# Optimization experiments

Measured on AMD Instinct MI355X. Metric: run time of the kernel, lower is better.

The kernel has to match this reference:

```python
import jax, jax.numpy as jnp
import numpy as np

GRID_SIZE = 10
DEGREE = 3


def bspline_basis(x, grid_size=GRID_SIZE, degree=DEGREE):
    """Cox-de Boor B-spline basis on a uniform grid over [-1, 1].
    x: (...,) -> (..., grid_size + degree)
    """
    h = 2.0 / grid_size
    # extended knot vector, length grid_size + 2*degree + 1
    knots = jnp.arange(-degree, grid_size + degree + 1, dtype=x.dtype) * h - 1.0
    # keep inputs inside the grid support (standard KAN practice)
    x = jnp.clip(x, -1.0, 1.0 - 1e-6)
    xe = x[..., None]
    b = ((xe >= knots[:-1]) & (xe < knots[1:])).astype(x.dtype)  # degree-0, (..., K-1)
    for d in range(1, degree + 1):
        left = (xe - knots[: -(d + 1)]) / (knots[d:-1] - knots[: -(d + 1)]) * b[..., :-1]
        right = (knots[d + 1:] - xe) / (knots[d + 1:] - knots[1:-d]) * b[..., 1:]
        b = left + right
    return b  # (..., grid_size + degree)


def setup_inputs() -> dict:
    key = jax.random.key(0)
    k1, k2, k3 = jax.random.split(key, 3)
    B, S, IN, OUT, E = 4, 2048, 256, 256, 8
    n_basis = GRID_SIZE + DEGREE
    x = jax.random.normal(k1, (B, S, IN), dtype=jnp.float32)
    coeff = jax.random.normal(k2, (E, n_basis), dtype=jnp.float32) * 0.1
    gating_weights = jax.random.normal(k3, (IN, OUT, E), dtype=jnp.float32)
    return {"x": x, "coeff": coeff, "gating_weights": gating_weights}


def reference(x, coeff, gating_weights):
    # spline experts: elementwise basis eval, then per-expert linear combo
    basis = bspline_basis(x)                              # (B, S, I, n_basis)
    expert_outputs = jnp.einsum('bsin,en->bsie', basis, coeff)  # (B, S, I, E)
    gates = jax.nn.softmax(gating_weights, axis=-1)       # (I, O, E)
    out = jnp.einsum('bsie,ioe->bso', expert_outputs, gates)
    return out
```

## Files before the change

kernel.cpp:

```cpp
#include <hip/hip_runtime.h>

typedef __attribute__((ext_vector_type(8))) short short8;
typedef __attribute__((ext_vector_type(4))) float f32x4;

#define IN_DIM 256
#define OUT_DIM 256
#define NB 16
#define KDIM (IN_DIM * NB)
#define TM 128
#define TN 128
#define BK 64
#define LDA 72
#define KSPLIT 2
#define IPER (IN_DIM / KSPLIT)
#define STEPS (IPER / 4)
#define XPITCH 129
#define XBYTES (TM * XPITCH * 4)
#define ABYTES (TM * LDA * 2)
#define LDS_TOTAL (XBYTES + 4 * ABYTES)

__device__ __forceinline__ unsigned short f2bf(float f) {
  union { float f; unsigned int u; } v; v.f = f;
  unsigned int r = v.u + 0x7fffu + ((v.u >> 16) & 1u);
  return (unsigned short)(r >> 16);
}

__device__ __forceinline__ void spline_row(float xv, unsigned short* rowp) {
  float xc = fminf(fmaxf(xv, -1.0f), 1.0f - 1e-6f);
  float u = (xc + 1.0f) * 5.0f;
  int c = (int)u;
  c = c > 9 ? 9 : (c < 0 ? 0 : c);
  float tt = u - (float)c;
  float omt = 1.0f - tt;
  float t2 = tt * tt, t3 = t2 * tt;
  float b0 = omt * omt * omt * (1.0f / 6.0f);
  float b1 = (3.0f * t3 - 6.0f * t2 + 4.0f) * (1.0f / 6.0f);
  float b2 = (-3.0f * t3 + 3.0f * t2 + 3.0f * tt + 1.0f) * (1.0f / 6.0f);
  float b3 = t3 * (1.0f / 6.0f);
  unsigned h0 = f2bf(b0), h1 = f2bf(b1), h2 = f2bf(b2), h3 = f2bf(b3);
  const int a = c >> 1;
  const bool odd = (c & 1) != 0;
  unsigned p01 = h0 | (h1 << 16);
  unsigned p23 = h2 | (h3 << 16);
  unsigned A0 = odd ? (h0 << 16) : p01;
  unsigned A1 = odd ? (h1 | (h2 << 16)) : p23;
  unsigned A2 = odd ? h3 : 0u;
  unsigned d[8];
#pragma unroll
  for (int j = 0; j < 8; ++j) {
    unsigned v = (j == a) ? A0 : 0u;
    v = (j == a + 1) ? A1 : v;
    v = (j == a + 2) ? A2 : v;
    d[j] = v;
  }
  *(int4*)&rowp[0] = *(const int4*)&d[0];
  *(int4*)&rowp[8] = *(const int4*)&d[4];
}

__global__ __launch_bounds__(256) void kan_prep(const float* __restrict__ coeff,
                                                const float* __restrict__ gw,
                                                unsigned short* __restrict__ BmT,
                                                float* __restrict__ out) {
  __shared__ float csh[104];
  __shared__ unsigned short tile[16][256];
  const int t = threadIdx.x;
  {
    const int bid = blockIdx.y * 16 + blockIdx.x;
    float4 z; z.x = z.y = z.z = z.w = 0.f;
    float4* ob = (float4*)out;
#pragma unroll
    for (int j = 0; j < 8; ++j) ob[(size_t)bid * 2048 + j * 256 + t] = z;
  }
  if (t < 104) csh[t] = coeff[t];
  __syncthreads();
  const int otile = blockIdx.x, itile = blockIdx.y;
  const int il = t >> 4, ol = t & 15;
  const int i = itile * 16 + il;
  const int o = otile * 16 + ol;
  const float* g = gw + (size_t)(i * OUT_DIM + o) * 8;
  float4 g0 = *(const float4*)g;
  float4 g1 = *(const float4*)(g + 4);
  float ge[8] = {g0.x, g0.y, g0.z, g0.w, g1.x, g1.y, g1.z, g1.w};
  float mx = ge[0];
#pragma unroll
  for (int e = 1; e < 8; ++e) mx = fmaxf(mx, ge[e]);
  float p[8]; float s = 0.f;
#pragma unroll
  for (int e = 0; e < 8; ++e) { p[e] = __expf(ge[e] - mx); s += p[e]; }
  const float inv = 1.0f / s;
  unsigned short row[16];
#pragma unroll
  for (int n = 0; n < 13; ++n) {
    float w = 0.f;
#pragma unroll
    for (int e = 0; e < 8; ++e) w += p[e] * csh[e * 13 + n];
    row[n] = f2bf(w * inv);
  }
  row[13] = 0; row[14] = 0; row[15] = 0;
  int4* dst = (int4*)&tile[ol][il * 16];
  dst[0] = *(const int4*)&row[0];
  dst[1] = *(const int4*)&row[8];
  __syncthreads();
  const int oo = t >> 4, ck = t & 15;
  int4 v0 = *(const int4*)&tile[oo][ck * 16];
  int4 v1 = *(const int4*)&tile[oo][ck * 16 + 8];
  int4* out4 = (int4*)(BmT + (size_t)(otile * 16 + oo) * KDIM + itile * 256 + ck * 16);
  out4[0] = v0;
  out4[1] = v1;
}

__global__ __launch_bounds__(256, 1) void kan_gemm(const float* __restrict__ x,
                                                   const unsigned short* __restrict__ BmT,
                                                   float* __restrict__ out) {
  extern __shared__ char lds_raw[];
  float* Xsh = (float*)lds_raw;
  unsigned short* AshB = (unsigned short*)(lds_raw + XBYTES);
  unsigned short* BshB = AshB + 2 * TM * LDA;

  const int t = threadIdx.x;
  const int lane = t & 63;
  const int wave = t >> 6;
  const int wm = wave & 1, wn = wave >> 1;
  const int mb = blockIdx.x * TM;
  const int ob = blockIdx.y * TN;
  const int i0 = blockIdx.z * IPER;

  const int mloc = t & 127;
  const int il0 = t >> 7;

  {
    const int xr = t >> 5;
    const int xc = t & 31;
#pragma unroll
    for (int p = 0; p < 16; ++p) {
      const int r = xr + 8 * p;
      float4 v = *(const float4*)(x + (size_t)(mb + r) * IN_DIM + i0 + xc * 4);
      float* d = Xsh + r * XPITCH + xc * 4;
      d[0] = v.x; d[1] = v.y; d[2] = v.z; d[3] = v.w;
    }
  }

  const unsigned short* bsrc[4];
  int bdst[4];
#pragma unroll
  for (int r = 0; r < 4; ++r) {
    int olo = (t >> 3) + 32 * r;
    bsrc[r] = BmT + (size_t)(ob + olo) * KDIM + i0 * NB + (t & 7) * 8;
    bdst[r] = olo * LDA + (t & 7) * 8;
  }

  int4 breg[4];
#pragma unroll
  for (int r = 0; r < 4; ++r) breg[r] = *(const int4*)(bsrc[r]);

  f32x4 acc[4][4];
#pragma unroll
  for (int a = 0; a < 4; ++a)
#pragma unroll
    for (int b = 0; b < 4; ++b) acc[a][b] = (f32x4){0.f, 0.f, 0.f, 0.f};

  int aoff[4], boff[4];
#pragma unroll
  for (int f = 0; f < 4; ++f) {
    aoff[f] = (wm * 64 + f * 16 + (lane & 15)) * LDA + (lane >> 4) * 8;
    boff[f] = (wn * 64 + f * 16 + (lane & 15)) * LDA + (lane >> 4) * 8;
  }

  __syncthreads();

  {
#pragma unroll
    for (int r = 0; r < 4; ++r) *(int4*)&BshB[bdst[r]] = breg[r];
#pragma unroll
    for (int rr = 0; rr < 2; ++rr) {
      const int il = il0 + 2 * rr;
      spline_row(Xsh[mloc * XPITCH + il], AshB + mloc * LDA + il * NB);
    }
  }

  for (int s = 0; s < STEPS; ++s) {
    __syncthreads();
    const int cur = s & 1;
    const bool more = (s + 1 < STEPS);
    if (more) {
#pragma unroll
      for (int r = 0; r < 4; ++r) breg[r] = *(const int4*)(bsrc[r] + (s + 1) * BK);
    }
    const unsigned short* Ac = AshB + cur * (TM * LDA);
    const unsigned short* Bc = BshB + cur * (TN * LDA);
#pragma unroll
    for (int kc = 0; kc < 2; ++kc) {
      short8 af[4], bfr[4];
#pragma unroll
      for (int f = 0; f < 4; ++f) af[f] = *(const short8*)&Ac[aoff[f] + kc * 32];
#pragma unroll
      for (int f = 0; f < 4; ++f) bfr[f] = *(const short8*)&Bc[boff[f] + kc * 32];
#pragma unroll
      for (int mf = 0; mf < 4; ++mf)
#pragma unroll
        for (int nf = 0; nf < 4; ++nf)
          acc[mf][nf] = __builtin_amdgcn_mfma_f32_16x16x32_bf16(af[mf], bfr[nf], acc[mf][nf], 0, 0, 0);
    }
    if (more) {
      unsigned short* An = AshB + (1 - cur) * (TM * LDA);
      unsigned short* Bn = BshB + (1 - cur) * (TN * LDA);
#pragma unroll
      for (int r = 0; r < 4; ++r) *(int4*)&Bn[bdst[r]] = breg[r];
#pragma unroll
      for (int rr = 0; rr < 2; ++rr) {
        const int il = il0 + 2 * rr;
        spline_row(Xsh[mloc * XPITCH + (s + 1) * 4 + il], An + mloc * LDA + il * NB);
      }
    }
  }

#pragma unroll
  for (int mf = 0; mf < 4; ++mf)
#pragma unroll
    for (int nf = 0; nf < 4; ++nf)
#pragma unroll
      for (int r = 0; r < 4; ++r) {
        int row = mb + wm * 64 + mf * 16 + ((lane >> 4) << 2) + r;
        int col = ob + wn * 64 + nf * 16 + (lane & 15);
        atomicAdd(out + (size_t)row * OUT_DIM + col, acc[mf][nf][r]);
      }
}

extern "C" void kernel_launch(void* const* d_in, const int* in_sizes, int n_in,
                              void* d_out, int out_size, void* d_ws, size_t ws_size,
                              hipStream_t stream) {
  const float* x     = (const float*)d_in[0];
  const float* coeff = (const float*)d_in[1];
  const float* gw    = (const float*)d_in[2];
  float* out = (float*)d_out;
  unsigned short* BmT = (unsigned short*)d_ws;

  hipFuncSetAttribute((const void*)kan_gemm,
                      hipFuncAttributeMaxDynamicSharedMemorySize, LDS_TOTAL);
  kan_prep<<<dim3(16, 16), dim3(256), 0, stream>>>(coeff, gw, BmT, out);
  dim3 grid(8192 / TM, OUT_DIM / TN, KSPLIT);
  kan_gemm<<<grid, dim3(256), LDS_TOTAL, stream>>>(x, BmT, out);
}
```

Measured before the change: 127.4 us.

## Drop LDS x staging, stream x per step, raise K-split and occupancy

Removes the large per-block shared-memory staging of x and instead loads two x values per thread from global memory each pipeline step, prefetched alongside the B tile. This shrinks LDS to the A/B double buffers only, which lets launch bounds request two blocks per CU. The K split is also doubled to 4 to create more blocks. The cost is more global atomics into the output and smaller, less coalesced per-step x loads.

```diff
diff --git a/kernel.cpp b/kernel.cpp
--- a/kernel.cpp
+++ b/kernel.cpp
@@ -11,13 +11,9 @@
 #define TN 128
 #define BK 64
 #define LDA 72
-#define KSPLIT 2
+#define KSPLIT 4
 #define IPER (IN_DIM / KSPLIT)
 #define STEPS (IPER / 4)
-#define XPITCH 129
-#define XBYTES (TM * XPITCH * 4)
-#define ABYTES (TM * LDA * 2)
-#define LDS_TOTAL (XBYTES + 4 * ABYTES)
 
 __device__ __forceinline__ unsigned short f2bf(float f) {
   union { float f; unsigned int u; } v; v.f = f;
@@ -109,13 +105,11 @@
   out4[1] = v1;
 }
 
-__global__ __launch_bounds__(256, 1) void kan_gemm(const float* __restrict__ x,
+__global__ __launch_bounds__(256, 2) void kan_gemm(const float* __restrict__ x,
                                                    const unsigned short* __restrict__ BmT,
                                                    float* __restrict__ out) {
-  extern __shared__ char lds_raw[];
-  float* Xsh = (float*)lds_raw;
-  unsigned short* AshB = (unsigned short*)(lds_raw + XBYTES);
-  unsigned short* BshB = AshB + 2 * TM * LDA;
+  __shared__ unsigned short AshB[2][TM * LDA];
+  __shared__ unsigned short BshB[2][TN * LDA];
 
   const int t = threadIdx.x;
   const int lane = t & 63;
@@ -125,33 +119,19 @@
   const int ob = blockIdx.y * TN;
   const int i0 = blockIdx.z * IPER;
 
-  const int mloc = t & 127;
-  const int il0 = t >> 7;
-
-  {
-    const int xr = t >> 5;
-    const int xc = t & 31;
-#pragma unroll
-    for (int p = 0; p < 16; ++p) {
-      const int r = xr + 8 * p;
-      float4 v = *(const float4*)(x + (size_t)(mb + r) * IN_DIM + i0 + xc * 4);
-      float* d = Xsh + r * XPITCH + xc * 4;
-      d[0] = v.x; d[1] = v.y; d[2] = v.z; d[3] = v.w;
-    }
-  }
+  const int r = t & 127;
+  const int ph = t >> 7;
+  const float* xrow = x + (size_t)(mb + r) * IN_DIM + i0 + 2 * ph;
+  const int adst = r * LDA + 2 * ph * NB;
 
   const unsigned short* bsrc[4];
   int bdst[4];
 #pragma unroll
-  for (int r = 0; r < 4; ++r) {
-    int olo = (t >> 3) + 32 * r;
-    bsrc[r] = BmT + (size_t)(ob + olo) * KDIM + i0 * NB + (t & 7) * 8;
-    bdst[r] = olo * LDA + (t & 7) * 8;
-  }
-
-  int4 breg[4];
-#pragma unroll
-  for (int r = 0; r < 4; ++r) breg[r] = *(const int4*)(bsrc[r]);
+  for (int q = 0; q < 4; ++q) {
+    int olo = (t >> 3) + 32 * q;
+    bsrc[q] = BmT + (size_t)(ob + olo) * KDIM + i0 * NB + (t & 7) * 8;
+    bdst[q] = olo * LDA + (t & 7) * 8;
+  }
 
   f32x4 acc[4][4];
 #pragma unroll
@@ -166,28 +146,30 @@
     boff[f] = (wn * 64 + f * 16 + (lane & 15)) * LDA + (lane >> 4) * 8;
   }
 
-  __syncthreads();
-
   {
-#pragma unroll
-    for (int r = 0; r < 4; ++r) *(int4*)&BshB[bdst[r]] = breg[r];
-#pragma unroll
-    for (int rr = 0; rr < 2; ++rr) {
-      const int il = il0 + 2 * rr;
-      spline_row(Xsh[mloc * XPITCH + il], AshB + mloc * LDA + il * NB);
-    }
+    float2 x0 = *(const float2*)xrow;
+    int4 breg[4];
+#pragma unroll
+    for (int q = 0; q < 4; ++q) breg[q] = *(const int4*)(bsrc[q]);
+#pragma unroll
+    for (int q = 0; q < 4; ++q) *(int4*)&BshB[0][bdst[q]] = breg[q];
+    spline_row(x0.x, &AshB[0][adst]);
+    spline_row(x0.y, &AshB[0][adst + NB]);
   }
 
   for (int s = 0; s < STEPS; ++s) {
     __syncthreads();
     const int cur = s & 1;
     const bool more = (s + 1 < STEPS);
+    int4 breg[4];
+    float2 xn;
     if (more) {
 #pragma unroll
-      for (int r = 0; r < 4; ++r) breg[r] = *(const int4*)(bsrc[r] + (s + 1) * BK);
+      for (int q = 0; q < 4; ++q) breg[q] = *(const int4*)(bsrc[q] + (s + 1) * BK);
+      xn = *(const float2*)(xrow + (s + 1) * 4);
     }
-    const unsigned short* Ac = AshB + cur * (TM * LDA);
-    const unsigned short* Bc = BshB + cur * (TN * LDA);
+    const unsigned short* Ac = AshB[cur];
+    const unsigned short* Bc = BshB[cur];
 #pragma unroll
     for (int kc = 0; kc < 2; ++kc) {
       short8 af[4], bfr[4];
@@ -202,15 +184,12 @@
           acc[mf][nf] = __builtin_amdgcn_mfma_f32_16x16x32_bf16(af[mf], bfr[nf], acc[mf][nf], 0, 0, 0);
     }
     if (more) {
-      unsigned short* An = AshB + (1 - cur) * (TM * LDA);
-      unsigned short* Bn = BshB + (1 - cur) * (TN * LDA);
-#pragma unroll
-      for (int r = 0; r < 4; ++r) *(int4*)&Bn[bdst[r]] = breg[r];
-#pragma unroll
-      for (int rr = 0; rr < 2; ++rr) {
-        const int il = il0 + 2 * rr;
-        spline_row(Xsh[mloc * XPITCH + (s + 1) * 4 + il], An + mloc * LDA + il * NB);
-      }
+      unsigned short* An = AshB[1 - cur];
+      unsigned short* Bn = BshB[1 - cur];
+#pragma unroll
+      for (int q = 0; q < 4; ++q) *(int4*)&Bn[bdst[q]] = breg[q];
+      spline_row(xn.x, An + adst);
+      spline_row(xn.y, An + adst + NB);
     }
   }
 
@@ -219,10 +198,10 @@
 #pragma unroll
     for (int nf = 0; nf < 4; ++nf)
 #pragma unroll
-      for (int r = 0; r < 4; ++r) {
-        int row = mb + wm * 64 + mf * 16 + ((lane >> 4) << 2) + r;
+      for (int q = 0; q < 4; ++q) {
+        int row = mb + wm * 64 + mf * 16 + ((lane >> 4) << 2) + q;
         int col = ob + wn * 64 + nf * 16 + (lane & 15);
-        atomicAdd(out + (size_t)row * OUT_DIM + col, acc[mf][nf][r]);
+        atomicAdd(out + (size_t)row * OUT_DIM + col, acc[mf][nf][q]);
       }
 }
 
@@ -235,9 +214,7 @@
   float* out = (float*)d_out;
   unsigned short* BmT = (unsigned short*)d_ws;
 
-  hipFuncSetAttribute((const void*)kan_gemm,
-                      hipFuncAttributeMaxDynamicSharedMemorySize, LDS_TOTAL);
   kan_prep<<<dim3(16, 16), dim3(256), 0, stream>>>(coeff, gw, BmT, out);
   dim3 grid(8192 / TM, OUT_DIM / TN, KSPLIT);
-  kan_gemm<<<grid, dim3(256), LDS_TOTAL, stream>>>(x, BmT, out);
-}
+  kan_gemm<<<grid, dim3(256), 0, stream>>>(x, BmT, out);
+}
```

Result: faster. 112.4 us (-11.7%).

## Build spline A-fragments in registers and raise K-split to four

Applied to the files above, without the earlier changes.

Each lane now builds its bf16 MFMA A-fragment directly in registers from x held in LDS. This removes the A-tile staging buffers, their LDS writes and reads, and the separate spline pass into LDS. The smaller LDS footprint allows two blocks per CU, and KSPLIT doubles to 4 for more parallelism, at the cost of twice as many output atomics and redundant spline evaluation, since each wave recomputes fragments for the rows it shares with the other N-wave. Bf16 packing now uses the HIP intrinsic, and the step loop is fully unrolled.

```diff
diff --git a/kernel.cpp b/kernel.cpp
--- a/kernel.cpp
+++ b/kernel.cpp
@@ -1,4 +1,5 @@
 #include <hip/hip_runtime.h>
+#include <hip/hip_bf16.h>
 
 typedef __attribute__((ext_vector_type(8))) short short8;
 typedef __attribute__((ext_vector_type(4))) float f32x4;
@@ -11,13 +12,13 @@
 #define TN 128
 #define BK 64
 #define LDA 72
-#define KSPLIT 2
+#define KSPLIT 4
 #define IPER (IN_DIM / KSPLIT)
 #define STEPS (IPER / 4)
-#define XPITCH 129
-#define XBYTES (TM * XPITCH * 4)
-#define ABYTES (TM * LDA * 2)
-#define LDS_TOTAL (XBYTES + 4 * ABYTES)
+#define XP 68
+#define XBYTES (TM * XP * 4)
+#define BBYTES (TN * LDA * 2)
+#define LDS_TOTAL (XBYTES + 2 * BBYTES)
 
 __device__ __forceinline__ unsigned short f2bf(float f) {
   union { float f; unsigned int u; } v; v.f = f;
@@ -25,7 +26,13 @@
   return (unsigned short)(r >> 16);
 }
 
-__device__ __forceinline__ void spline_row(float xv, unsigned short* rowp) {
+__device__ __forceinline__ unsigned pk2(float lo, float hi) {
+  union { __hip_bfloat162 h; unsigned u; } cv;
+  cv.h = __float22bfloat162_rn(make_float2(lo, hi));
+  return cv.u;
+}
+
+__device__ __forceinline__ short8 make_afrag(float xv, int iq) {
   float xc = fminf(fmaxf(xv, -1.0f), 1.0f - 1e-6f);
   float u = (xc + 1.0f) * 5.0f;
   int c = (int)u;
@@ -37,24 +44,24 @@
   float b1 = (3.0f * t3 - 6.0f * t2 + 4.0f) * (1.0f / 6.0f);
   float b2 = (-3.0f * t3 + 3.0f * t2 + 3.0f * tt + 1.0f) * (1.0f / 6.0f);
   float b3 = t3 * (1.0f / 6.0f);
-  unsigned h0 = f2bf(b0), h1 = f2bf(b1), h2 = f2bf(b2), h3 = f2bf(b3);
+  unsigned p01 = pk2(b0, b1), p23 = pk2(b2, b3);
+  unsigned q0 = pk2(0.0f, b0), q12 = pk2(b1, b2), q3 = pk2(b3, 0.0f);
+  const bool odd = (c & 1) != 0;
   const int a = c >> 1;
-  const bool odd = (c & 1) != 0;
-  unsigned p01 = h0 | (h1 << 16);
-  unsigned p23 = h2 | (h3 << 16);
-  unsigned A0 = odd ? (h0 << 16) : p01;
-  unsigned A1 = odd ? (h1 | (h2 << 16)) : p23;
-  unsigned A2 = odd ? h3 : 0u;
-  unsigned d[8];
-#pragma unroll
-  for (int j = 0; j < 8; ++j) {
-    unsigned v = (j == a) ? A0 : 0u;
-    v = (j == a + 1) ? A1 : v;
-    v = (j == a + 2) ? A2 : v;
-    d[j] = v;
-  }
-  *(int4*)&rowp[0] = *(const int4*)&d[0];
-  *(int4*)&rowp[8] = *(const int4*)&d[4];
+  unsigned A0 = odd ? q0 : p01;
+  unsigned A1 = odd ? q12 : p23;
+  unsigned A2 = odd ? q3 : 0u;
+  union { unsigned u4[4]; short8 v; } r;
+  const int base = iq * 4;
+#pragma unroll
+  for (int j = 0; j < 4; ++j) {
+    int d = base + j - a;
+    unsigned v = (d == 0) ? A0 : 0u;
+    v = (d == 1) ? A1 : v;
+    v = (d == 2) ? A2 : v;
+    r.u4[j] = v;
+  }
+  return r.v;
 }
 
 __global__ __launch_bounds__(256) void kan_prep(const float* __restrict__ coeff,
@@ -109,13 +116,12 @@
   out4[1] = v1;
 }
 
-__global__ __launch_bounds__(256, 1) void kan_gemm(const float* __restrict__ x,
+__global__ __launch_bounds__(256, 2) void kan_gemm(const float* __restrict__ x,
                                                    const unsigned short* __restrict__ BmT,
                                                    float* __restrict__ out) {
   extern __shared__ char lds_raw[];
   float* Xsh = (float*)lds_raw;
-  unsigned short* AshB = (unsigned short*)(lds_raw + XBYTES);
-  unsigned short* BshB = AshB + 2 * TM * LDA;
+  unsigned short* BshB = (unsigned short*)(lds_raw + XBYTES);
 
   const int t = threadIdx.x;
   const int lane = t & 63;
@@ -125,18 +131,18 @@
   const int ob = blockIdx.y * TN;
   const int i0 = blockIdx.z * IPER;
 
-  const int mloc = t & 127;
-  const int il0 = t >> 7;
+  const int lrow = lane & 15;
+  const int q = lane >> 4;
+  const int iq = q & 1;
+  const int ih = q >> 1;
 
   {
-    const int xr = t >> 5;
-    const int xc = t & 31;
-#pragma unroll
-    for (int p = 0; p < 16; ++p) {
-      const int r = xr + 8 * p;
-      float4 v = *(const float4*)(x + (size_t)(mb + r) * IN_DIM + i0 + xc * 4);
-      float* d = Xsh + r * XPITCH + xc * 4;
-      d[0] = v.x; d[1] = v.y; d[2] = v.z; d[3] = v.w;
+#pragma unroll
+    for (int j = 0; j < 8; ++j) {
+      const int id = j * 256 + t;
+      const int row = id >> 4, c4 = id & 15;
+      float4 v = *(const float4*)(x + (size_t)(mb + row) * IN_DIM + i0 + c4 * 4);
+      *(float4*)(Xsh + row * XP + c4 * 4) = v;
     }
   }
 
@@ -149,50 +155,46 @@
     bdst[r] = olo * LDA + (t & 7) * 8;
   }
 
-  int4 breg[4];
-#pragma unroll
-  for (int r = 0; r < 4; ++r) breg[r] = *(const int4*)(bsrc[r]);
-
   f32x4 acc[4][4];
 #pragma unroll
   for (int a = 0; a < 4; ++a)
 #pragma unroll
     for (int b = 0; b < 4; ++b) acc[a][b] = (f32x4){0.f, 0.f, 0.f, 0.f};
 
-  int aoff[4], boff[4];
-#pragma unroll
-  for (int f = 0; f < 4; ++f) {
-    aoff[f] = (wm * 64 + f * 16 + (lane & 15)) * LDA + (lane >> 4) * 8;
-    boff[f] = (wn * 64 + f * 16 + (lane & 15)) * LDA + (lane >> 4) * 8;
+  int boff[4];
+#pragma unroll
+  for (int f = 0; f < 4; ++f)
+    boff[f] = (wn * 64 + f * 16 + lrow) * LDA + q * 8;
+
+  {
+    int4 breg[4];
+#pragma unroll
+    for (int r = 0; r < 4; ++r) breg[r] = *(const int4*)(bsrc[r]);
+#pragma unroll
+    for (int r = 0; r < 4; ++r) *(int4*)&BshB[bdst[r]] = breg[r];
   }
 
   __syncthreads();
 
-  {
-#pragma unroll
-    for (int r = 0; r < 4; ++r) *(int4*)&BshB[bdst[r]] = breg[r];
-#pragma unroll
-    for (int rr = 0; rr < 2; ++rr) {
-      const int il = il0 + 2 * rr;
-      spline_row(Xsh[mloc * XPITCH + il], AshB + mloc * LDA + il * NB);
-    }
-  }
-
+#pragma unroll
   for (int s = 0; s < STEPS; ++s) {
-    __syncthreads();
     const int cur = s & 1;
     const bool more = (s + 1 < STEPS);
+    int4 breg[4];
     if (more) {
 #pragma unroll
       for (int r = 0; r < 4; ++r) breg[r] = *(const int4*)(bsrc[r] + (s + 1) * BK);
     }
-    const unsigned short* Ac = AshB + cur * (TM * LDA);
     const unsigned short* Bc = BshB + cur * (TN * LDA);
 #pragma unroll
     for (int kc = 0; kc < 2; ++kc) {
+      const int xcol = s * 4 + kc * 2 + ih;
       short8 af[4], bfr[4];
 #pragma unroll
-      for (int f = 0; f < 4; ++f) af[f] = *(const short8*)&Ac[aoff[f] + kc * 32];
+      for (int mf = 0; mf < 4; ++mf) {
+        float xv = Xsh[(wm * 64 + mf * 16 + lrow) * XP + xcol];
+        af[mf] = make_afrag(xv, iq);
+      }
 #pragma unroll
       for (int f = 0; f < 4; ++f) bfr[f] = *(const short8*)&Bc[boff[f] + kc * 32];
 #pragma unroll
@@ -202,16 +204,11 @@
           acc[mf][nf] = __builtin_amdgcn_mfma_f32_16x16x32_bf16(af[mf], bfr[nf], acc[mf][nf], 0, 0, 0);
     }
     if (more) {
-      unsigned short* An = AshB + (1 - cur) * (TM * LDA);
       unsigned short* Bn = BshB + (1 - cur) * (TN * LDA);
 #pragma unroll
       for (int r = 0; r < 4; ++r) *(int4*)&Bn[bdst[r]] = breg[r];
-#pragma unroll
-      for (int rr = 0; rr < 2; ++rr) {
-        const int il = il0 + 2 * rr;
-        spline_row(Xsh[mloc * XPITCH + (s + 1) * 4 + il], An + mloc * LDA + il * NB);
-      }
-    }
+    }
+    __syncthreads();
   }
 
 #pragma unroll
@@ -220,8 +217,8 @@
     for (int nf = 0; nf < 4; ++nf)
 #pragma unroll
       for (int r = 0; r < 4; ++r) {
-        int row = mb + wm * 64 + mf * 16 + ((lane >> 4) << 2) + r;
-        int col = ob + wn * 64 + nf * 16 + (lane & 15);
+        int row = mb + wm * 64 + mf * 16 + (q << 2) + r;
+        int col = ob + wn * 64 + nf * 16 + lrow;
         atomicAdd(out + (size_t)row * OUT_DIM + col, acc[mf][nf][r]);
       }
 }
```

New measurement: 133.9 us. 1.05x slower.
